# Kernel tuning notes

Measured on AMD Instinct MI355X. Metric: run time of the kernel, lower is better.

Reference implementation:

```python
import jax, jax.numpy as jnp
import numpy as np

IMG_SIZE = 640.0
CONF_THRESH = 0.001
NMS_THRESH = 0.6
TOP_K = 1000  # fixed-shape candidate cap per class


def _pairwise_iou(b):
    # b: [K,4] in x1,y1,x2,y2; replicates the numpy NMS math (1e-28 / 1e-14 eps)
    x1, y1, x2, y2 = b[:, 0], b[:, 1], b[:, 2], b[:, 3]
    areas = (x2 - x1) * (y2 - y1)
    xx1 = jnp.maximum(x1[:, None], x1[None, :])
    yy1 = jnp.maximum(y1[:, None], y1[None, :])
    xx2 = jnp.minimum(x2[:, None], x2[None, :])
    yy2 = jnp.minimum(y2[:, None], y2[None, :])
    w = jnp.maximum(1e-28, xx2 - xx1)
    h = jnp.maximum(1e-28, yy2 - yy1)
    inter = w * h
    return inter / (areas[:, None] + areas[None, :] - inter + 1e-14)


def setup_inputs() -> dict:
    key = jax.random.key(0)
    k1, k2, k3 = jax.random.split(key, 3)
    img_size, strides, KA, C = 640, [8, 16, 32], 3, 80
    anchor = np.array([[10, 13], [16, 30], [33, 23], [30, 61], [62, 45], [59, 119],
                       [116, 90], [156, 198], [373, 326]], np.float32).reshape(3, 3, 2)
    grids, anchs, strs = [], [], []
    for lvl, s in enumerate(strides):
        f = img_size // s
        gy, gx = np.meshgrid(np.arange(f), np.arange(f), indexing='ij')
        gxy = np.stack([gx, gy], -1).reshape(-1, 1, 2).astype(np.float32)
        grids.append(np.broadcast_to(gxy, (f * f, KA, 2)).reshape(-1, 2))
        anchs.append(np.broadcast_to(anchor[lvl][None], (f * f, KA, 2)).reshape(-1, 2).astype(np.float32))
        strs.append(np.full((f * f * KA, 1), s, np.float32))
    grid_xy = jnp.asarray(np.concatenate(grids, 0))      # [N,2]
    anchors_wh = jnp.asarray(np.concatenate(anchs, 0))   # [N,2]
    stride_t = jnp.asarray(np.concatenate(strs, 0))      # [N,1]
    N = grid_xy.shape[0]  # 25200
    return {
        'reg_pred': jax.random.normal(k1, (N, 4), jnp.float32),
        'obj_pred': jax.random.normal(k2, (N, 1), jnp.float32),
        'cls_pred': jax.random.normal(k3, (N, C), jnp.float32),
        'grid_xy': grid_xy,
        'anchors_wh': anchors_wh,
        'stride_t': stride_t,
    }


def reference(reg_pred, obj_pred, cls_pred, grid_xy, anchors_wh, stride_t):
    # ---- box decode (YOLO head) ----
    xy = (jax.nn.sigmoid(reg_pred[:, :2]) + grid_xy) * stride_t       # centers in pixels
    wh = jnp.exp(reg_pred[:, 2:]) * anchors_wh                        # sizes in pixels
    boxes = jnp.concatenate([xy - 0.5 * wh, xy + 0.5 * wh], axis=-1)  # [N,4]
    boxes = jnp.clip(boxes / IMG_SIZE, 0.0, 1.0)
    # ---- scoring: sigmoid(obj) * softmax(cls) ----
    scores_all = jax.nn.sigmoid(obj_pred) * jax.nn.softmax(cls_pred, axis=-1)  # [N,C]
    cls_inds = jnp.argmax(scores_all, axis=-1)          # [N]
    scores = jnp.max(scores_all, axis=-1)               # [N]
    C = cls_pred.shape[-1]
    K = TOP_K
    ar = jnp.arange(K)

    def nms_class(c):
        s_c = jnp.where((cls_inds == c) & (scores >= CONF_THRESH), scores, -1.0)
        vals, idx = jax.lax.top_k(s_c, K)               # sorted desc, fixed shape
        b = boxes[idx]                                  # [K,4]
        valid = vals > 0.0
        iou = _pairwise_iou(b)                          # [K,K]

        def body(i, keep):
            sup = keep[i] & (iou[i] > NMS_THRESH) & (ar > i)
            return keep & ~sup

        keep = jax.lax.fori_loop(0, K, body, valid)
        return b, vals, keep

    boxes_out, scores_out, keep = jax.vmap(nms_class)(jnp.arange(C))  # [C,K,4],[C,K],[C,K]
    return boxes_out, scores_out * keep.astype(scores_out.dtype), keep
```

## Files before the change

kernel.cpp:

```cpp
#include <hip/hip_runtime.h>
#include <cstdint>
#include <cstddef>

#define N_CLS 80
#define TOPK 1000
#define POOL_N 2048
#define MCAP 512
#define BD 1024
#define DTB2 1024
#define NBLK 25
#define SLICE 128
#define LDSB_STRIDE 10

__global__ __launch_bounds__(DTB2) void decode_kernel(
    const float* __restrict__ reg, const float* __restrict__ obj,
    const float* __restrict__ cls, const float* __restrict__ grid,
    const float* __restrict__ anch, const float* __restrict__ strd,
    float* __restrict__ boxes, uint2* __restrict__ scs,
    int* __restrict__ cnts, uint2* __restrict__ gpool2, int N) {
  __shared__ int hcnt[N_CLS];
  const int blk = blockIdx.x;
  const int tid = threadIdx.x;
  const int i = blk * DTB2 + tid;

  if (tid < N_CLS) hcnt[tid] = 0;
  __syncthreads();

  const bool valid = (i < N);
  float best = -1.0f;
  int bc = 0;

  if (valid) {
    const float4 r = ((const float4*)reg)[i];
    const float2 g = ((const float2*)grid)[i];
    const float2 aw = ((const float2*)anch)[i];
    const float st = strd[i];

    float cx = (1.0f / (1.0f + expf(-r.x)) + g.x) * st;
    float cy = (1.0f / (1.0f + expf(-r.y)) + g.y) * st;
    float w = expf(r.z) * aw.x;
    float h = expf(r.w) * aw.y;
    float b0 = fminf(fmaxf((cx - 0.5f * w) / 640.0f, 0.0f), 1.0f);
    float b1 = fminf(fmaxf((cy - 0.5f * h) / 640.0f, 0.0f), 1.0f);
    float b2 = fminf(fmaxf((cx + 0.5f * w) / 640.0f, 0.0f), 1.0f);
    float b3 = fminf(fmaxf((cy + 0.5f * h) / 640.0f, 0.0f), 1.0f);
    float4 bo; bo.x = b0; bo.y = b1; bo.z = b2; bo.w = b3;
    ((float4*)boxes)[i] = bo;

    const float4* cr = (const float4*)cls + (size_t)i * 20;
    float4 x[20];
#pragma unroll
    for (int q = 0; q < 20; ++q) x[q] = cr[q];

    float4 m4 = x[0];
#pragma unroll
    for (int q = 1; q < 20; ++q) {
      m4.x = fmaxf(m4.x, x[q].x); m4.y = fmaxf(m4.y, x[q].y);
      m4.z = fmaxf(m4.z, x[q].z); m4.w = fmaxf(m4.w, x[q].w);
    }
    float mx = fmaxf(fmaxf(m4.x, m4.y), fmaxf(m4.z, m4.w));

#pragma unroll
    for (int q = 0; q < 20; ++q) {
      x[q].x = expf(x[q].x - mx); x[q].y = expf(x[q].y - mx);
      x[q].z = expf(x[q].z - mx); x[q].w = expf(x[q].w - mx);
    }

    float s = 0.0f;
#pragma unroll
    for (int q = 0; q < 20; ++q) {
      s += x[q].x; s += x[q].y; s += x[q].z; s += x[q].w;
    }

    float sig = 1.0f / (1.0f + expf(-obj[i]));

#pragma unroll
    for (int q = 0; q < 20; ++q) {
      float q0 = sig * (x[q].x / s);
      if (q0 > best) { best = q0; bc = 4 * q + 0; }
      float q1 = sig * (x[q].y / s);
      if (q1 > best) { best = q1; bc = 4 * q + 1; }
      float q2 = sig * (x[q].z / s);
      if (q2 > best) { best = q2; bc = 4 * q + 2; }
      float q3 = sig * (x[q].w / s);
      if (q3 > best) { best = q3; bc = 4 * q + 3; }
    }
    scs[i] = make_uint2(__float_as_uint(best), (unsigned)bc);
  }

  const bool pos = valid && (best >= 0.001f);
  int slot = -1;
  if (pos) slot = atomicAdd(&hcnt[bc], 1);
  __syncthreads();
  if (tid < N_CLS) cnts[tid * NBLK + blk] = min(hcnt[tid], SLICE);
  if (pos && slot < SLICE)
    gpool2[((size_t)bc * NBLK + blk) * SLICE + slot] =
        make_uint2(__float_as_uint(best), (unsigned)i);
}

__device__ __forceinline__ unsigned long long kinit(int w, int m) {
  int lo = w << 6;
  return (m <= lo) ? 0ULL : ((m - lo >= 64) ? ~0ULL : ((1ULL << (m - lo)) - 1ULL));
}

__global__ __launch_bounds__(BD) void nms_kernel(
    const float* __restrict__ boxes, const uint2* __restrict__ scs,
    const int* __restrict__ cnts, const uint2* __restrict__ gpool2,
    float* __restrict__ out, int N) {
  const int c = blockIdx.x;
  const int tid = threadIdx.x;

  __shared__ uint2 pool[POOL_N];
  __shared__ float svals[TOPK];
  __shared__ int sidx[TOPK];
  __shared__ __align__(16) float4 bxyz[TOPK];
  __shared__ __align__(16) unsigned long long ldsB[MCAP * LDSB_STRIDE];
  __shared__ unsigned char kp[TOPK];
  __shared__ __align__(16) unsigned long long kmbuf[2][8];
  __shared__ int wsum[BD / 64 + 1];
  __shared__ int pref[NBLK + 1];

  if (tid == 0) {
    int acc = 0;
    pref[0] = 0;
    const int* cc = cnts + c * NBLK;
#pragma unroll
    for (int b = 0; b < NBLK; ++b) {
      acc = min(acc + cc[b], POOL_N);
      pref[b + 1] = acc;
    }
  }
  __syncthreads();
  const int cnt = pref[NBLK];
  const int m = min(cnt, TOPK);

  const uint2* gp = gpool2 + (size_t)c * NBLK * SLICE;
  for (int t = tid; t < cnt; t += BD) {
    int b = 0;
#pragma unroll
    for (int q = 0; q < NBLK; ++q) b += (int)(t >= pref[q + 1]);
    pool[t] = gp[(size_t)b * SLICE + (t - pref[b])];
  }
  __syncthreads();

  for (int e = tid; e < cnt; e += BD) {
    uint2 me = pool[e];
    float v = __uint_as_float(me.x);
    int idx = (int)me.y;
    int r = 0;
#pragma unroll 8
    for (int k = 0; k < cnt; ++k) {
      uint2 q = pool[k];
      float vk = __uint_as_float(q.x);
      r += (int)((vk > v) || (vk == v && (int)q.y < idx));
    }
    if (r < TOPK) { svals[r] = v; sidx[r] = idx; }
  }
  __syncthreads();

  const int M = TOPK - m;
  if (M > 0) {
    int i = tid;
    bool f = false;
    if (i < N) {
      uint2 sc = scs[i];
      f = !((int)sc.y == c && __uint_as_float(sc.x) >= 0.001f);
    }
    unsigned long long mk = __ballot(f ? 1 : 0);
    int lane = tid & 63, wv = tid >> 6;
    int pre = __popcll(mk & ((1ULL << lane) - 1ULL));
    if (lane == 0) wsum[wv] = __popcll(mk);
    __syncthreads();
    if (tid == 0) {
      int acc = 0;
      for (int wq = 0; wq < BD / 64; ++wq) { int t2 = wsum[wq]; wsum[wq] = acc; acc += t2; }
    }
    __syncthreads();
    int pos = wsum[wv] + pre;
    if (f && pos < M) sidx[m + pos] = i;
  }
  __syncthreads();

  const float4* bf4 = (const float4*)boxes;
  for (int t = tid; t < TOPK; t += BD) bxyz[t] = bf4[sidx[t]];
  __syncthreads();

  const int W = (m + 63) >> 6;
  const bool fast = (m > 0) && (m <= MCAP);
  int cur = 0;

  if (fast) {
    const int tasks = m * W;
    for (int q = tid; q < tasks; q += BD) {
      int w = q / m;
      int j = q - w * m;
      unsigned long long bits = 0ULL;
      if (w <= (j >> 6)) {
        float4 jb = bxyz[j];
        float aj = (jb.z - jb.x) * (jb.w - jb.y);
        int i0 = w << 6, iend = min(i0 + 64, j);
        for (int i = i0; i < iend; ++i) {
          float4 ib = bxyz[i];
          float ai = (ib.z - ib.x) * (ib.w - ib.y);
          float xx1 = fmaxf(ib.x, jb.x), yy1 = fmaxf(ib.y, jb.y);
          float xx2 = fminf(ib.z, jb.z), yy2 = fminf(ib.w, jb.w);
          float ww = fmaxf(1e-28f, xx2 - xx1), hh = fmaxf(1e-28f, yy2 - yy1);
          float inter = ww * hh;
          float iou = inter / (ai + aj - inter + 1e-14f);
          if (iou > 0.6f) bits |= (1ULL << (i - i0));
        }
      }
      ldsB[(size_t)j * LDSB_STRIDE + w] = bits;
    }
    __syncthreads();

    ulonglong2 ta, tb, tc, td;
    ta = tb = tc = td = make_ulonglong2(0ULL, 0ULL);
    if (tid < m) {
      const ulonglong2* rp = (const ulonglong2*)&ldsB[(size_t)tid * LDSB_STRIDE];
      ta = rp[0]; tb = rp[1]; tc = rp[2]; td = rp[3];
    }
    if (tid < 8) kmbuf[0][tid] = kinit(tid, m);
    __syncthreads();

    for (;;) {
      bool keep = false;
      if (tid < m) {
        unsigned long long sup =
            (ta.x & kmbuf[cur][0]) | (ta.y & kmbuf[cur][1]) |
            (tb.x & kmbuf[cur][2]) | (tb.y & kmbuf[cur][3]) |
            (tc.x & kmbuf[cur][4]) | (tc.y & kmbuf[cur][5]) |
            (td.x & kmbuf[cur][6]) | (td.y & kmbuf[cur][7]);
        keep = (sup == 0ULL);
      }
      bool old = (tid < m) &&
                 ((kmbuf[cur][tid >> 6] >> (tid & 63)) & 1ULL);
      unsigned long long bl = __ballot(keep ? 1 : 0);
      int wv = tid >> 6;
      if ((tid & 63) == 0 && wv < 8) kmbuf[cur ^ 1][wv] = bl;
      int any = __syncthreads_or((int)(keep != old));
      cur ^= 1;
      if (!any) break;
    }
  } else {
    for (int t = tid; t < TOPK; t += BD) kp[t] = (t < m) ? 1 : 0;
    __syncthreads();
    for (int i = 0; i < m; ++i) {
      if (kp[i]) {
        float4 rb = bxyz[i];
        float ai = (rb.z - rb.x) * (rb.w - rb.y);
        for (int j = i + 1 + tid; j < m; j += BD) {
          if (kp[j]) {
            float4 jb = bxyz[j];
            float aj = (jb.z - jb.x) * (jb.w - jb.y);
            float xx1 = fmaxf(rb.x, jb.x), yy1 = fmaxf(rb.y, jb.y);
            float xx2 = fminf(rb.z, jb.z), yy2 = fminf(rb.w, jb.w);
            float ww = fmaxf(1e-28f, xx2 - xx1), hh = fmaxf(1e-28f, yy2 - yy1);
            float inter = ww * hh;
            float iou = inter / (ai + aj - inter + 1e-14f);
            if (iou > 0.6f) kp[j] = 0;
          }
        }
      }
      __syncthreads();
    }
  }

  float* outB = out;
  float* outS = out + N_CLS * TOPK * 4;
  float* outK = outS + N_CLS * TOPK;
  for (int t = tid; t < TOPK; t += BD) {
    float k = 0.0f;
    if (t < m)
      k = fast ? (float)((kmbuf[cur][t >> 6] >> (t & 63)) & 1ULL)
               : (float)kp[t];
    float v = (t < m) ? svals[t] : -1.0f;
    ((float4*)outB)[c * TOPK + t] = bxyz[t];
    outS[c * TOPK + t] = v * k;
    outK[c * TOPK + t] = k;
  }
}

extern "C" void kernel_launch(void* const* d_in, const int* in_sizes, int n_in,
                              void* d_out, int out_size, void* d_ws, size_t ws_size,
                              hipStream_t stream) {
  const float* reg  = (const float*)d_in[0];
  const float* obj  = (const float*)d_in[1];
  const float* cls  = (const float*)d_in[2];
  const float* grid = (const float*)d_in[3];
  const float* anch = (const float*)d_in[4];
  const float* strd = (const float*)d_in[5];
  const int N = in_sizes[0] / 4;

  char* w8 = (char*)d_ws;
  size_t off = 0;
  float* boxes  = (float*)(w8 + off); off += (size_t)N * 16;
  uint2* scs    = (uint2*)(w8 + off); off += (size_t)N * 8;
  int*   cnts   = (int*)(w8 + off);   off += (size_t)N_CLS * NBLK * 4;
  uint2* gpool2 = (uint2*)(w8 + off); off += (size_t)N_CLS * NBLK * SLICE * 8;
  float* out = (float*)d_out;

  decode_kernel<<<NBLK, DTB2, 0, stream>>>(
      reg, obj, cls, grid, anch, strd, boxes, scs, cnts, gpool2, N);
  nms_kernel<<<N_CLS, BD, 0, stream>>>(boxes, scs, cnts, gpool2, out, N);
}
```

Before: 124.6 us.

## Use many small decode blocks with wave-parallel prefix scan and binary-search pool gather

The decode kernel goes from 25 blocks of 1024 threads to 197 blocks of 128 threads, spreading the per-class work over many more CUs, and the per-block class slice shrinks to 32 entries. To cope with the much larger block count, the NMS kernel now builds its per-class prefix over block counts with a 64-lane shuffle scan instead of a serial single-thread loop, and gathers pool entries with a binary search instead of a linear scan. The risk is that 32 slots per block per class could overflow for a dense class, and the extra per-block slices make the gather more scattered.

After: 113.6 us. -8.8%, faster.

```diff
diff --git a/kernel.cpp b/kernel.cpp
--- a/kernel.cpp
+++ b/kernel.cpp
@@ -7,12 +7,12 @@
 #define POOL_N 2048
 #define MCAP 512
 #define BD 1024
-#define DTB2 1024
-#define NBLK 25
-#define SLICE 128
+#define DTB 128
+#define NBLK 197
+#define SLICE 32
 #define LDSB_STRIDE 10
 
-__global__ __launch_bounds__(DTB2) void decode_kernel(
+__global__ __launch_bounds__(DTB) void decode_kernel(
     const float* __restrict__ reg, const float* __restrict__ obj,
     const float* __restrict__ cls, const float* __restrict__ grid,
     const float* __restrict__ anch, const float* __restrict__ strd,
@@ -21,7 +21,7 @@
   __shared__ int hcnt[N_CLS];
   const int blk = blockIdx.x;
   const int tid = threadIdx.x;
-  const int i = blk * DTB2 + tid;
+  const int i = blk * DTB + tid;
 
   if (tid < N_CLS) hcnt[tid] = 0;
   __syncthreads();
@@ -120,14 +120,20 @@
   __shared__ int wsum[BD / 64 + 1];
   __shared__ int pref[NBLK + 1];
 
-  if (tid == 0) {
-    int acc = 0;
-    pref[0] = 0;
+  if (tid < 64) {
     const int* cc = cnts + c * NBLK;
-#pragma unroll
-    for (int b = 0; b < NBLK; ++b) {
-      acc = min(acc + cc[b], POOL_N);
-      pref[b + 1] = acc;
+    int carry = 0;
+    if (tid == 0) pref[0] = 0;
+    for (int ch = 0; ch < (NBLK + 63) / 64; ++ch) {
+      int b = ch * 64 + tid;
+      int v = (b < NBLK) ? cc[b] : 0;
+#pragma unroll
+      for (int s = 1; s < 64; s <<= 1) {
+        int u = __shfl_up(v, s, 64);
+        if (tid >= (unsigned)s) v += u;
+      }
+      if (b < NBLK) pref[b + 1] = min(carry + v, POOL_N);
+      carry += __shfl(v, 63, 64);
     }
   }
   __syncthreads();
@@ -136,10 +142,12 @@
 
   const uint2* gp = gpool2 + (size_t)c * NBLK * SLICE;
   for (int t = tid; t < cnt; t += BD) {
-    int b = 0;
-#pragma unroll
-    for (int q = 0; q < NBLK; ++q) b += (int)(t >= pref[q + 1]);
-    pool[t] = gp[(size_t)b * SLICE + (t - pref[b])];
+    int lo = 0, hi = NBLK;
+    while (hi - lo > 1) {
+      int mid = (lo + hi) >> 1;
+      if (t >= pref[mid]) lo = mid; else hi = mid;
+    }
+    pool[t] = gp[(size_t)lo * SLICE + (t - pref[lo])];
   }
   __syncthreads();
 
@@ -300,7 +308,7 @@
   uint2* gpool2 = (uint2*)(w8 + off); off += (size_t)N_CLS * NBLK * SLICE * 8;
   float* out = (float*)d_out;
 
-  decode_kernel<<<NBLK, DTB2, 0, stream>>>(
+  decode_kernel<<<NBLK, DTB, 0, stream>>>(
       reg, obj, cls, grid, anch, strd, boxes, scs, cnts, gpool2, N);
   nms_kernel<<<N_CLS, BD, 0, stream>>>(boxes, scs, cnts, gpool2, out, N);
 }
```
